# Kernel tuning notes

Hardware: AMD Instinct MI355X
Metric: run time of the kernel (lower is better)

The kernel has to match this reference:

```python
import jax, jax.numpy as jnp
import numpy as np


def hadamard_matrix(n):
    # Sylvester construction; n must be a power of 2.
    H = np.array([[1.0]], dtype=np.float32)
    while H.shape[0] < n:
        H = np.block([[H, H], [H, -H]])
    return H


def setup_inputs() -> dict:
    key = jax.random.key(0)
    k1, k2, k3 = jax.random.split(key, 3)
    B, C, Hh, Ww, P = 8, 64, 256, 256, 4
    x = jax.random.normal(k1, (B, C, Hh, Ww), dtype=jnp.float32)
    v = jax.random.uniform(k2, (P, Hh, Ww), dtype=jnp.float32)          # torch.rand init
    T = jax.random.uniform(k3, (P, Hh, Ww), dtype=jnp.float32) / 10.0   # torch.rand/10 init
    return {"x": x, "v": v, "T": T}


def _wht2d(u, Hm, sc):
    # normalized Walsh-Hadamard transform along last two axes (H symmetric)
    u = jnp.einsum('...hw,vw->...hv', u, Hm) * sc   # axis=-1
    u = jnp.einsum('...hv,gh->...gv', u, Hm) * sc   # axis=-2
    return u


def reference(x, v, T):
    n = x.shape[-1]  # 256, power of 2; height_pad==height so no padding
    Hm = jnp.asarray(hadamard_matrix(n), dtype=x.dtype)
    sc = jnp.asarray(1.0 / np.sqrt(n), dtype=x.dtype)
    f2 = _wht2d(x, Hm, sc)                              # (B,C,H,W)
    a = f2[None] * v[:, None, None]                     # (P,B,C,H,W)
    st = jnp.tanh(a) * jax.nn.relu(jnp.abs(a) - jnp.abs(T)[:, None, None])
    f6 = st.sum(axis=0)                                 # (B,C,H,W)
    f8 = _wht2d(f6, Hm, sc)
    return f8 + x                                       # residual=True
```

## Files before the change

kernel.cpp:

```cpp
#include <hip/hip_runtime.h>
#include <hip/hip_fp16.h>


#define NPX 65536
#define SC  0.0625f

__device__ __forceinline__ unsigned int h2u(__half2 h) {
  union { __half2 h; unsigned int u; } c; c.h = h; return c.u;
}
__device__ __forceinline__ __half2 u2h(unsigned int u) {
  union { __half2 h; unsigned int u; } c; c.u = u; return c.h;
}

__device__ __forceinline__ void fwht16(float f[16]) {
  #pragma unroll
  for (int d = 1; d < 16; d <<= 1) {
    #pragma unroll
    for (int i = 0; i < 16; ++i) {
      if (!(i & d)) {
        float a = f[i], b = f[i | d];
        f[i]     = a + b;
        f[i | d] = a - b;
      }
    }
  }
}

__device__ __forceinline__ void fwht256_wave(float r[4], int lane) {
  float a0 = r[0] + r[1], b0 = r[0] - r[1];
  float a1 = r[2] + r[3], b1 = r[2] - r[3];
  r[0] = a0 + a1; r[1] = b0 + b1; r[2] = a0 - a1; r[3] = b0 - b1;
  #pragma unroll
  for (int m = 1; m <= 32; m <<= 1) {
    const float s = (lane & m) ? -1.0f : 1.0f;
    #pragma unroll
    for (int j = 0; j < 4; ++j) {
      float t = __shfl_xor(r[j], m);
      r[j] = fmaf(r[j], s, t);
    }
  }
}

__device__ __forceinline__ float g_term(float a, float absT) {
  float ax = fabsf(a);
  float rl = fmaxf(ax - absT, 0.0f);
  float e  = __builtin_amdgcn_exp2f(ax * 2.8853900817779268f);
  float th = 1.0f - 2.0f * __builtin_amdgcn_rcpf(e + 1.0f);
  return copysignf(th, a) * rl;
}

__global__ __launch_bounds__(1024) void k_fused(const float* __restrict__ x,
                                                const float* __restrict__ v,
                                                const float* __restrict__ T,
                                                float* __restrict__ out) {
  __shared__ __half S[256 * 256];
  const int tid  = threadIdx.x;
  const int lane = tid & 63;
  const int wv   = tid >> 6;
  const size_t pbase = (size_t)blockIdx.x * NPX;

  #pragma unroll 2
  for (int rr = 0; rr < 16; ++rr) {
    const int row = wv * 16 + rr;
    const float4 xv = *reinterpret_cast<const float4*>(x + pbase + (size_t)row * 256 + 4 * lane);
    float r[4] = {xv.x, xv.y, xv.z, xv.w};
    fwht256_wave(r, lane);
    uint2 pk;
    pk.x = h2u(__floats2half2_rn(r[0] * SC, r[1] * SC));
    pk.y = h2u(__floats2half2_rn(r[2] * SC, r[3] * SC));
    *reinterpret_cast<uint2*>(&S[row * 256 + 4 * lane]) = pk;
  }
  __syncthreads();

  const int q = tid & 63;
  const int g = tid >> 6;
  const int c   = tid & 255;
  const int grp = tid >> 8;
  float fp[2][16];

  #pragma unroll 1
  for (int hs = 0; hs < 2; ++hs) {
    const int cb = 2 * q + 128 * hs;
    #pragma unroll
    for (int k = 0; k < 16; ++k) {
      unsigned int d = *reinterpret_cast<unsigned int*>(&S[(16 * g + k) * 256 + cb]);
      float2 e = __half22float2(u2h(d));
      fp[0][k] = e.x; fp[1][k] = e.y;
    }
    fwht16(fp[0]); fwht16(fp[1]);
    #pragma unroll
    for (int k = 0; k < 16; ++k) {
      *reinterpret_cast<unsigned int*>(&S[(16 * g + k) * 256 + cb]) =
          h2u(__floats2half2_rn(fp[0][k], fp[1][k]));
    }
  }
  __syncthreads();

  {
    float f[16];
    #pragma unroll 1
    for (int gg = grp; gg < 16; gg += 4) {
      #pragma unroll
      for (int a = 0; a < 16; ++a)
        f[a] = __half2float(S[(gg + 16 * a) * 256 + c]);
      fwht16(f);
      #pragma unroll
      for (int a = 0; a < 16; ++a) f[a] *= SC;

      #pragma unroll 2
      for (int a = 0; a < 16; ++a) {
        const int off = (gg + 16 * a) * 256 + c;
        float acc = 0.f;
        #pragma unroll
        for (int p = 0; p < 4; ++p)
          acc += g_term(f[a] * v[p * NPX + off], fabsf(T[p * NPX + off]));
        f[a] = acc;
      }

      fwht16(f);
      #pragma unroll
      for (int a = 0; a < 16; ++a)
        S[(gg + 16 * a) * 256 + c] = __float2half_rn(f[a] * SC);
    }
  }
  __syncthreads();

  #pragma unroll 1
  for (int hs = 0; hs < 2; ++hs) {
    const int cb = 2 * q + 128 * hs;
    #pragma unroll
    for (int k = 0; k < 16; ++k) {
      unsigned int d = *reinterpret_cast<unsigned int*>(&S[(16 * g + k) * 256 + cb]);
      float2 e = __half22float2(u2h(d));
      fp[0][k] = e.x; fp[1][k] = e.y;
    }
    fwht16(fp[0]); fwht16(fp[1]);
    #pragma unroll
    for (int k = 0; k < 16; ++k) {
      *reinterpret_cast<unsigned int*>(&S[(16 * g + k) * 256 + cb]) =
          h2u(__floats2half2_rn(fp[0][k], fp[1][k]));
    }
  }
  __syncthreads();

  #pragma unroll 2
  for (int rr = 0; rr < 16; ++rr) {
    const int row = wv * 16 + rr;
    uint2 pk = *reinterpret_cast<uint2*>(&S[row * 256 + 4 * lane]);
    float2 lo = __half22float2(u2h(pk.x));
    float2 hi = __half22float2(u2h(pk.y));
    float r[4] = {lo.x, lo.y, hi.x, hi.y};
    fwht256_wave(r, lane);
    const float4 xv = *reinterpret_cast<const float4*>(x + pbase + (size_t)row * 256 + 4 * lane);
    float4 o;
    o.x = fmaf(r[0], SC, xv.x);
    o.y = fmaf(r[1], SC, xv.y);
    o.z = fmaf(r[2], SC, xv.z);
    o.w = fmaf(r[3], SC, xv.w);
    *reinterpret_cast<float4*>(out + pbase + (size_t)row * 256 + 4 * lane) = o;
  }
}

extern "C" void kernel_launch(void* const* d_in, const int* in_sizes, int n_in,
                              void* d_out, int out_size, void* d_ws, size_t ws_size,
                              hipStream_t stream) {
  const float* x = (const float*)d_in[0];
  const float* v = (const float*)d_in[1];
  const float* T = (const float*)d_in[2];
  float* out = (float*)d_out;

  k_fused<<<512, 1024, 0, stream>>>(x, v, T, out);
}
```

Before: 171.1 us.

## Split fused kernel into row-transform, column/threshold, and inverse-row kernels

Replaces the single kernel that kept a whole 256x256 fp16 plane in 128KB of LDS per 1024-thread block with three kernels. A row-FWHT kernel writes fp16 to workspace. A mid kernel does the column transforms and soft-threshold on 64-column slices using 32KB of LDS. A final row-FWHT kernel adds the residual. The aim is higher occupancy and more parallel blocks than one block per plane allows, at the cost of an extra fp16 round trip through global memory and two more launches. g_term is also simplified to use signed exp for tanh instead of copysign.

```diff
diff --git a/kernel.cpp b/kernel.cpp
--- a/kernel.cpp
+++ b/kernel.cpp
@@ -2,8 +2,9 @@
 #include <hip/hip_fp16.h>
 
 
-#define NPX 65536
-#define SC  0.0625f
+#define NPX   65536
+#define NROWS (512 * 256)
+#define SC    0.0625f
 
 __device__ __forceinline__ unsigned int h2u(__half2 h) {
   union { __half2 h; unsigned int u; } c; c.h = h; return c.u;
@@ -42,74 +43,73 @@
 }
 
 __device__ __forceinline__ float g_term(float a, float absT) {
-  float ax = fabsf(a);
-  float rl = fmaxf(ax - absT, 0.0f);
-  float e  = __builtin_amdgcn_exp2f(ax * 2.8853900817779268f);
+  float e  = __builtin_amdgcn_exp2f(a * 2.8853900817779268f);
   float th = 1.0f - 2.0f * __builtin_amdgcn_rcpf(e + 1.0f);
-  return copysignf(th, a) * rl;
+  float rl = fmaxf(fabsf(a) - absT, 0.0f);
+  return th * rl;
 }
 
-__global__ __launch_bounds__(1024) void k_fused(const float* __restrict__ x,
-                                                const float* __restrict__ v,
-                                                const float* __restrict__ T,
-                                                float* __restrict__ out) {
-  __shared__ __half S[256 * 256];
-  const int tid  = threadIdx.x;
-  const int lane = tid & 63;
-  const int wv   = tid >> 6;
-  const size_t pbase = (size_t)blockIdx.x * NPX;
-
-  #pragma unroll 2
-  for (int rr = 0; rr < 16; ++rr) {
-    const int row = wv * 16 + rr;
-    const float4 xv = *reinterpret_cast<const float4*>(x + pbase + (size_t)row * 256 + 4 * lane);
+__global__ __launch_bounds__(256) void k_rowf(const float* __restrict__ x,
+                                              __half* __restrict__ t1) {
+  const int lane = threadIdx.x & 63;
+  const int wave = blockIdx.x * 4 + (threadIdx.x >> 6);
+  const int nw   = gridDim.x * 4;
+  for (int row = wave; row < NROWS; row += nw) {
+    const float4 xv = *reinterpret_cast<const float4*>(x + (size_t)row * 256 + 4 * lane);
     float r[4] = {xv.x, xv.y, xv.z, xv.w};
     fwht256_wave(r, lane);
     uint2 pk;
     pk.x = h2u(__floats2half2_rn(r[0] * SC, r[1] * SC));
     pk.y = h2u(__floats2half2_rn(r[2] * SC, r[3] * SC));
-    *reinterpret_cast<uint2*>(&S[row * 256 + 4 * lane]) = pk;
+    *reinterpret_cast<uint2*>(t1 + (size_t)row * 256 + 4 * lane) = pk;
   }
-  __syncthreads();
+}
 
-  const int q = tid & 63;
-  const int g = tid >> 6;
-  const int c   = tid & 255;
-  const int grp = tid >> 8;
-  float fp[2][16];
+__global__ __launch_bounds__(512) void k_mid(__half* __restrict__ t1,
+                                             const float* __restrict__ v,
+                                             const float* __restrict__ T) {
+  __shared__ __half S[256 * 64];
+  const int tid = threadIdx.x;
+  const int plane = blockIdx.x >> 2;
+  const int w0    = (blockIdx.x & 3) * 64;
+  __half* tp = t1 + (size_t)plane * NPX + w0;
 
-  #pragma unroll 1
-  for (int hs = 0; hs < 2; ++hs) {
-    const int cb = 2 * q + 128 * hs;
+  {
+    const int cp = tid & 31;
+    const int g  = tid >> 5;
+    float fA[16], fB[16];
     #pragma unroll
     for (int k = 0; k < 16; ++k) {
-      unsigned int d = *reinterpret_cast<unsigned int*>(&S[(16 * g + k) * 256 + cb]);
-      float2 e = __half22float2(u2h(d));
-      fp[0][k] = e.x; fp[1][k] = e.y;
+      const unsigned int d =
+          *reinterpret_cast<const unsigned int*>(tp + (16 * g + k) * 256 + 2 * cp);
+      const float2 e = __half22float2(u2h(d));
+      fA[k] = e.x; fB[k] = e.y;
     }
-    fwht16(fp[0]); fwht16(fp[1]);
+    fwht16(fA); fwht16(fB);
     #pragma unroll
-    for (int k = 0; k < 16; ++k) {
-      *reinterpret_cast<unsigned int*>(&S[(16 * g + k) * 256 + cb]) =
-          h2u(__floats2half2_rn(fp[0][k], fp[1][k]));
-    }
+    for (int k = 0; k < 16; ++k)
+      *reinterpret_cast<unsigned int*>(&S[(16 * g + k) * 64 + 2 * cp]) =
+          h2u(__floats2half2_rn(fA[k], fB[k]));
   }
   __syncthreads();
 
   {
+    const int c   = tid & 63;
+    const int grp = tid >> 6;
     float f[16];
     #pragma unroll 1
-    for (int gg = grp; gg < 16; gg += 4) {
+    for (int s = 0; s < 2; ++s) {
+      const int gg = grp + 8 * s;
       #pragma unroll
       for (int a = 0; a < 16; ++a)
-        f[a] = __half2float(S[(gg + 16 * a) * 256 + c]);
+        f[a] = __half2float(S[(gg + 16 * a) * 64 + c]);
       fwht16(f);
       #pragma unroll
       for (int a = 0; a < 16; ++a) f[a] *= SC;
 
-      #pragma unroll 2
+      #pragma unroll 4
       for (int a = 0; a < 16; ++a) {
-        const int off = (gg + 16 * a) * 256 + c;
+        const int off = (gg + 16 * a) * 256 + w0 + c;
         float acc = 0.f;
         #pragma unroll
         for (int p = 0; p < 4; ++p)
@@ -120,44 +120,48 @@
       fwht16(f);
       #pragma unroll
       for (int a = 0; a < 16; ++a)
-        S[(gg + 16 * a) * 256 + c] = __float2half_rn(f[a] * SC);
+        S[(gg + 16 * a) * 64 + c] = __float2half_rn(f[a] * SC);
     }
   }
   __syncthreads();
 
-  #pragma unroll 1
-  for (int hs = 0; hs < 2; ++hs) {
-    const int cb = 2 * q + 128 * hs;
+  {
+    const int cp = tid & 31;
+    const int g  = tid >> 5;
+    float fA[16], fB[16];
     #pragma unroll
     for (int k = 0; k < 16; ++k) {
-      unsigned int d = *reinterpret_cast<unsigned int*>(&S[(16 * g + k) * 256 + cb]);
-      float2 e = __half22float2(u2h(d));
-      fp[0][k] = e.x; fp[1][k] = e.y;
+      const float2 e = __half22float2(
+          u2h(*reinterpret_cast<unsigned int*>(&S[(16 * g + k) * 64 + 2 * cp])));
+      fA[k] = e.x; fB[k] = e.y;
     }
-    fwht16(fp[0]); fwht16(fp[1]);
+    fwht16(fA); fwht16(fB);
     #pragma unroll
-    for (int k = 0; k < 16; ++k) {
-      *reinterpret_cast<unsigned int*>(&S[(16 * g + k) * 256 + cb]) =
-          h2u(__floats2half2_rn(fp[0][k], fp[1][k]));
-    }
+    for (int k = 0; k < 16; ++k)
+      *reinterpret_cast<unsigned int*>(tp + (16 * g + k) * 256 + 2 * cp) =
+          h2u(__floats2half2_rn(fA[k], fB[k]));
   }
-  __syncthreads();
+}
 
-  #pragma unroll 2
-  for (int rr = 0; rr < 16; ++rr) {
-    const int row = wv * 16 + rr;
-    uint2 pk = *reinterpret_cast<uint2*>(&S[row * 256 + 4 * lane]);
-    float2 lo = __half22float2(u2h(pk.x));
-    float2 hi = __half22float2(u2h(pk.y));
+__global__ __launch_bounds__(256) void k_rowb(const __half* __restrict__ t1,
+                                              const float* __restrict__ x,
+                                              float* __restrict__ out) {
+  const int lane = threadIdx.x & 63;
+  const int wave = blockIdx.x * 4 + (threadIdx.x >> 6);
+  const int nw   = gridDim.x * 4;
+  for (int row = wave; row < NROWS; row += nw) {
+    const uint2 pk = *reinterpret_cast<const uint2*>(t1 + (size_t)row * 256 + 4 * lane);
+    const float2 lo = __half22float2(u2h(pk.x));
+    const float2 hi = __half22float2(u2h(pk.y));
     float r[4] = {lo.x, lo.y, hi.x, hi.y};
     fwht256_wave(r, lane);
-    const float4 xv = *reinterpret_cast<const float4*>(x + pbase + (size_t)row * 256 + 4 * lane);
+    const float4 xv = *reinterpret_cast<const float4*>(x + (size_t)row * 256 + 4 * lane);
     float4 o;
     o.x = fmaf(r[0], SC, xv.x);
     o.y = fmaf(r[1], SC, xv.y);
     o.z = fmaf(r[2], SC, xv.z);
     o.w = fmaf(r[3], SC, xv.w);
-    *reinterpret_cast<float4*>(out + pbase + (size_t)row * 256 + 4 * lane) = o;
+    *reinterpret_cast<float4*>(out + (size_t)row * 256 + 4 * lane) = o;
   }
 }
 
@@ -168,6 +172,9 @@
   const float* v = (const float*)d_in[1];
   const float* T = (const float*)d_in[2];
   float* out = (float*)d_out;
+  __half* t1 = (__half*)d_ws;
 
-  k_fused<<<512, 1024, 0, stream>>>(x, v, T, out);
+  k_rowf<<<2048, 256, 0, stream>>>(x, t1);
+  k_mid <<<2048, 512, 0, stream>>>(t1, v, T);
+  k_rowb<<<2048, 256, 0, stream>>>(t1, x, out);
 }
```

New measurement: 192.4 us. +12.5%, slower.
